# Kernel optimization log

Measured on AMD Instinct MI355X. Metric: run time of the kernel, lower is better.

## Reference

```python
import jax, jax.numpy as jnp
import numpy as np

BETA = 0.25


def setup_inputs() -> dict:
    key = jax.random.key(0)
    k1, k2 = jax.random.split(key)
    z_e = jax.random.normal(k1, (32, 64, 64, 64), dtype=jnp.float32)  # [B, C, W, H]
    # nn.Embedding weight initialized uniform(-1, 1)
    emb = jax.random.uniform(k2, (1024, 64), dtype=jnp.float32, minval=-1.0, maxval=1.0)
    return {"z_e": z_e, "emb": emb}


def reference(z_e, emb):
    B, C, W, H = z_e.shape
    # [B, C, W, H] -> [B, W, H, C] -> [N, C]
    z = jnp.transpose(z_e, (0, 2, 3, 1))
    z_flat = z.reshape(-1, C)  # [N, C]
    # squared euclidean distances: ||z||^2 + ||e||^2 - 2 z e^T  -> [N, K]
    d = (jnp.sum(z_flat ** 2, axis=1, keepdims=True)
         + jnp.sum(emb ** 2, axis=1)
         - 2.0 * jnp.matmul(z_flat, emb.T))
    indices = jnp.argmin(d, axis=1)  # [N]
    quantized = emb[indices].reshape(z.shape)  # [B, W, H, C]
    vq_loss = (jnp.mean((jax.lax.stop_gradient(quantized) - z) ** 2)
               + BETA * jnp.mean((quantized - jax.lax.stop_gradient(z)) ** 2))
    quantized = jnp.transpose(quantized, (0, 3, 1, 2))  # [B, C, W, H]
    return quantized, indices, vq_loss
```

## Files before the change

### kernel.cpp

```cpp
#include <hip/hip_runtime.h>


#define CDIM   64
#define KCODES 1024
#define NPTS   131072
#define WH     4096
#define CWH    262144
#define CTILES (KCODES / 16)
#define DELTA  0.008f

typedef __attribute__((ext_vector_type(4))) float f32x4;
typedef __attribute__((ext_vector_type(8))) short bf16x8;
typedef __attribute__((ext_vector_type(8))) unsigned short u16x8;

__device__ inline unsigned short f2bf(float f) {
    unsigned u = __float_as_uint(f);
    return (unsigned short)((u + 0x7FFFu + ((u >> 16) & 1u)) >> 16);
}
__device__ inline float bf2f(unsigned short h) {
    return __uint_as_float(((unsigned)h) << 16);
}

__global__ __launch_bounds__(256) void vq_prep(const float* __restrict__ emb,
                                               unsigned short* __restrict__ e_swz,
                                               float* __restrict__ E,
                                               int* __restrict__ cnt) {
    const int id = blockIdx.x * 256 + threadIdx.x;
    if (id == 0) cnt[0] = 0;

    if (id < KCODES) {
        const int c = id;
        const float4* e4 = (const float4*)(emb + c * CDIM);
        float s = 0.f;
#pragma unroll
        for (int i = 0; i < CDIM / 4; ++i) {
            float4 v = e4[i];
            s = fmaf(v.x, v.x, s); s = fmaf(v.y, v.y, s);
            s = fmaf(v.z, v.z, s); s = fmaf(v.w, v.w, s);
        }
        E[c] = s;
    }

    if (id < KCODES * 8) {
        const int c  = id >> 3;
        const int kh = (id >> 2) & 1;
        const int g  = id & 3;
        const int ct = c >> 4, col = c & 15;
        const int lane = (g << 4) | col;
        const size_t bh = ((size_t)(ct * 2 + 0) * 2 + kh) * 512 + (size_t)lane * 8;
        const size_t bl = ((size_t)(ct * 2 + 1) * 2 + kh) * 512 + (size_t)lane * 8;
        u16x8 his, los;
#pragma unroll
        for (int j = 0; j < 8; ++j) {
            float v = emb[c * CDIM + kh * 32 + g * 8 + j];
            unsigned short hi = f2bf(v);
            unsigned short lo = f2bf(v - bf2f(hi));
            his[j] = hi;
            los[j] = lo;
        }
        *(u16x8*)&e_swz[bh] = his;
        *(u16x8*)&e_swz[bl] = los;
    }
}

__global__ __launch_bounds__(256) void vq_scan_mfma(const float* __restrict__ z_e,
                                                    const unsigned short* __restrict__ e_swz,
                                                    const float* __restrict__ E,
                                                    int* __restrict__ bestk,
                                                    int* __restrict__ list,
                                                    int* __restrict__ cnt) {
    const int tid = threadIdx.x;
    const int n0  = blockIdx.x * 128;
    const int b   = n0 >> 12;
    const int wh0 = n0 & 4095;

    __shared__ unsigned short zfrag[8][2][2][512];

    const float* zp = z_e + (size_t)b * CWH + wh0;
#pragma unroll 4
    for (int i = 0; i < 32; ++i) {
        int flat = i * 256 + tid;
        int c = flat >> 7, p = flat & 127;
        float v = zp[(size_t)c * WH + p];
        unsigned short hi = f2bf(v);
        unsigned short lo = f2bf(v - bf2f(hi));
        int slot = ((((c & 31) >> 3) << 4) | (p & 15)) * 8 + (c & 7);
        zfrag[p >> 4][0][c >> 5][slot] = hi;
        zfrag[p >> 4][1][c >> 5][slot] = lo;
    }
    __syncthreads();

    const int lane = tid & 63;
    const int w    = tid >> 6;

    bf16x8 zf[2][2][2];
#pragma unroll
    for (int pt = 0; pt < 2; ++pt)
#pragma unroll
        for (int s = 0; s < 2; ++s)
#pragma unroll
            for (int kh = 0; kh < 2; ++kh)
                zf[pt][s][kh] = *(const bf16x8*)&zfrag[2 * w + pt][s][kh][lane * 8];

    const bf16x8* ebv = (const bf16x8*)e_swz;
    const int eoff = ((lane >> 4) << 2);

    float m1a[4], m2a[4], m1b[4], m2b[4];
    int   k1a[4], k1b[4];
#pragma unroll
    for (int i = 0; i < 4; ++i) {
        m1a[i] = 1e30f; m2a[i] = 1e30f; k1a[i] = 0;
        m1b[i] = 1e30f; m2b[i] = 1e30f; k1b[i] = 0;
    }

    bf16x8 eh0 = ebv[0 * 64 + lane];
    bf16x8 eh1 = ebv[1 * 64 + lane];
    bf16x8 el0 = ebv[2 * 64 + lane];
    bf16x8 el1 = ebv[3 * 64 + lane];
    f32x4  Ev  = *(const f32x4*)(E + eoff);

    for (int ct = 0; ct < CTILES; ++ct) {
        const int ctn = (ct + 1) & 63;
        bf16x8 p0 = ebv[(ctn * 4 + 0) * 64 + lane];
        bf16x8 p1 = ebv[(ctn * 4 + 1) * 64 + lane];
        bf16x8 p2 = ebv[(ctn * 4 + 2) * 64 + lane];
        bf16x8 p3 = ebv[(ctn * 4 + 3) * 64 + lane];
        f32x4  Ep = *(const f32x4*)(E + ctn * 16 + eoff);

        f32x4 acc0 = {0.f, 0.f, 0.f, 0.f};
        f32x4 acc1 = {0.f, 0.f, 0.f, 0.f};
        acc0 = __builtin_amdgcn_mfma_f32_16x16x32_bf16(eh0, zf[0][0][0], acc0, 0, 0, 0);
        acc0 = __builtin_amdgcn_mfma_f32_16x16x32_bf16(eh1, zf[0][0][1], acc0, 0, 0, 0);
        acc0 = __builtin_amdgcn_mfma_f32_16x16x32_bf16(eh0, zf[0][1][0], acc0, 0, 0, 0);
        acc0 = __builtin_amdgcn_mfma_f32_16x16x32_bf16(eh1, zf[0][1][1], acc0, 0, 0, 0);
        acc0 = __builtin_amdgcn_mfma_f32_16x16x32_bf16(el0, zf[0][0][0], acc0, 0, 0, 0);
        acc0 = __builtin_amdgcn_mfma_f32_16x16x32_bf16(el1, zf[0][0][1], acc0, 0, 0, 0);
        acc1 = __builtin_amdgcn_mfma_f32_16x16x32_bf16(eh0, zf[1][0][0], acc1, 0, 0, 0);
        acc1 = __builtin_amdgcn_mfma_f32_16x16x32_bf16(eh1, zf[1][0][1], acc1, 0, 0, 0);
        acc1 = __builtin_amdgcn_mfma_f32_16x16x32_bf16(eh0, zf[1][1][0], acc1, 0, 0, 0);
        acc1 = __builtin_amdgcn_mfma_f32_16x16x32_bf16(eh1, zf[1][1][1], acc1, 0, 0, 0);
        acc1 = __builtin_amdgcn_mfma_f32_16x16x32_bf16(el0, zf[1][0][0], acc1, 0, 0, 0);
        acc1 = __builtin_amdgcn_mfma_f32_16x16x32_bf16(el1, zf[1][0][1], acc1, 0, 0, 0);

        const int kb = ct * 16 + eoff;
#pragma unroll
        for (int i = 0; i < 4; ++i) {
            float s0 = fmaf(-2.0f, acc0[i], Ev[i]);
            if (s0 < m1a[i]) { m2a[i] = m1a[i]; m1a[i] = s0; k1a[i] = kb + i; }
            else             { m2a[i] = fminf(m2a[i], s0); }
            float s1 = fmaf(-2.0f, acc1[i], Ev[i]);
            if (s1 < m1b[i]) { m2b[i] = m1b[i]; m1b[i] = s1; k1b[i] = kb + i; }
            else             { m2b[i] = fminf(m2b[i], s1); }
        }

        eh0 = p0; eh1 = p1; el0 = p2; el1 = p3; Ev = Ep;
    }

    float m1A = m1a[0], m2A = m2a[0]; int k1A = k1a[0];
    float m1B = m1b[0], m2B = m2b[0]; int k1B = k1b[0];
#pragma unroll
    for (int i = 1; i < 4; ++i) {
        bool take = (m1a[i] < m1A) || (m1a[i] == m1A && k1a[i] < k1A);
        float nm2 = take ? fminf(m1A, m2a[i]) : fminf(m2A, m1a[i]);
        if (take) { m1A = m1a[i]; k1A = k1a[i]; }
        m2A = nm2;
        take = (m1b[i] < m1B) || (m1b[i] == m1B && k1b[i] < k1B);
        nm2 = take ? fminf(m1B, m2b[i]) : fminf(m2B, m1b[i]);
        if (take) { m1B = m1b[i]; k1B = k1b[i]; }
        m2B = nm2;
    }

#pragma unroll
    for (int d = 16; d <= 32; d <<= 1) {
        float om1 = __shfl_xor(m1A, d); int ok1 = __shfl_xor(k1A, d); float om2 = __shfl_xor(m2A, d);
        bool take = (om1 < m1A) || (om1 == m1A && ok1 < k1A);
        float nm2 = take ? fminf(m1A, om2) : fminf(m2A, om1);
        if (take) { m1A = om1; k1A = ok1; }
        m2A = nm2;
        om1 = __shfl_xor(m1B, d); ok1 = __shfl_xor(k1B, d); om2 = __shfl_xor(m2B, d);
        take = (om1 < m1B) || (om1 == m1B && ok1 < k1B);
        nm2 = take ? fminf(m1B, om2) : fminf(m2B, om1);
        if (take) { m1B = om1; k1B = ok1; }
        m2B = nm2;
    }

    if (lane < 16) {
        int na  = n0 + (2 * w + 0) * 16 + lane;
        int nb_ = n0 + (2 * w + 1) * 16 + lane;
        bestk[na]  = k1A;
        bestk[nb_] = k1B;
        if (m2A - m1A <= DELTA) { int p = atomicAdd(cnt, 1); list[p] = na; }
        if (m2B - m1B <= DELTA) { int p = atomicAdd(cnt, 1); list[p] = nb_; }
    }
}

__global__ __launch_bounds__(256) void vq_rescue(const float* __restrict__ z_e,
                                                 const float* __restrict__ emb,
                                                 const float* __restrict__ E,
                                                 const int* __restrict__ list,
                                                 const int* __restrict__ cnt,
                                                 int* __restrict__ bestk) {
    const int total  = cnt[0];
    const int lane   = threadIdx.x & 63;
    const int wid    = (blockIdx.x * 256 + threadIdx.x) >> 6;
    const int nwaves = (gridDim.x * 256) >> 6;

    for (int i = wid; i < total; i += nwaves) {
        const int n  = list[i];
        const int b  = n >> 12, wh = n & 4095;
        const float* zp = z_e + (size_t)b * CWH + wh;
        float z[CDIM];
#pragma unroll
        for (int c = 0; c < CDIM; ++c) z[c] = zp[c * WH];

        float best = 1e30f; int bk = 0;
        const int kbase = lane * 16;
#pragma unroll 4
        for (int j = 0; j < 16; ++j) {
            const int k = kbase + j;
            const float4* er4 = (const float4*)(emb + k * CDIM);
            float d0 = 0.f, d1 = 0.f, d2 = 0.f, d3 = 0.f;
#pragma unroll
            for (int c4 = 0; c4 < CDIM / 4; ++c4) {
                float4 v = er4[c4];
                d0 = fmaf(z[4 * c4 + 0], v.x, d0);
                d1 = fmaf(z[4 * c4 + 1], v.y, d1);
                d2 = fmaf(z[4 * c4 + 2], v.z, d2);
                d3 = fmaf(z[4 * c4 + 3], v.w, d3);
            }
            float dot   = (d0 + d1) + (d2 + d3);
            float score = fmaf(-2.0f, dot, E[k]);
            if (score < best) { best = score; bk = k; }
        }
#pragma unroll
        for (int d = 1; d < 64; d <<= 1) {
            float ob = __shfl_xor(best, d);
            int   ok = __shfl_xor(bk, d);
            if (ob < best || (ob == best && ok < bk)) { best = ob; bk = ok; }
        }
        if (lane == 0) bestk[n] = bk;
    }
}

__global__ __launch_bounds__(256) void vq_merge(const float* __restrict__ z_e,
                                                const float* __restrict__ emb,
                                                const int* __restrict__ kf,
                                                float* __restrict__ out_q,
                                                float* __restrict__ out_idx,
                                                float* __restrict__ partials) {
    const int tid = threadIdx.x;
    const int cq  = tid >> 5;
    const int pq  = tid & 31;
    const int n0  = blockIdx.x * 128 + pq * 4;
    const int b   = n0 >> 12;
    const int wh  = n0 & 4095;

    const int4 mk4 = *(const int4*)&kf[n0];
    if (cq == 0) {
        float4 fx = { (float)mk4.x, (float)mk4.y, (float)mk4.z, (float)mk4.w };
        *(float4*)&out_idx[n0] = fx;
    }

    const int c0 = cq * 8;
    float4 e0a = *(const float4*)&emb[mk4.x * CDIM + c0];
    float4 e0b = *(const float4*)&emb[mk4.x * CDIM + c0 + 4];
    float4 e1a = *(const float4*)&emb[mk4.y * CDIM + c0];
    float4 e1b = *(const float4*)&emb[mk4.y * CDIM + c0 + 4];
    float4 e2a = *(const float4*)&emb[mk4.z * CDIM + c0];
    float4 e2b = *(const float4*)&emb[mk4.z * CDIM + c0 + 4];
    float4 e3a = *(const float4*)&emb[mk4.w * CDIM + c0];
    float4 e3b = *(const float4*)&emb[mk4.w * CDIM + c0 + 4];

    float qv[8][4];
    qv[0][0] = e0a.x; qv[0][1] = e1a.x; qv[0][2] = e2a.x; qv[0][3] = e3a.x;
    qv[1][0] = e0a.y; qv[1][1] = e1a.y; qv[1][2] = e2a.y; qv[1][3] = e3a.y;
    qv[2][0] = e0a.z; qv[2][1] = e1a.z; qv[2][2] = e2a.z; qv[2][3] = e3a.z;
    qv[3][0] = e0a.w; qv[3][1] = e1a.w; qv[3][2] = e2a.w; qv[3][3] = e3a.w;
    qv[4][0] = e0b.x; qv[4][1] = e1b.x; qv[4][2] = e2b.x; qv[4][3] = e3b.x;
    qv[5][0] = e0b.y; qv[5][1] = e1b.y; qv[5][2] = e2b.y; qv[5][3] = e3b.y;
    qv[6][0] = e0b.z; qv[6][1] = e1b.z; qv[6][2] = e2b.z; qv[6][3] = e3b.z;
    qv[7][0] = e0b.w; qv[7][1] = e1b.w; qv[7][2] = e2b.w; qv[7][3] = e3b.w;

    const float* zb = z_e   + (size_t)b * CWH + wh;
    float*       qb = out_q + (size_t)b * CWH + wh;
    float lsum = 0.f;
#pragma unroll
    for (int cc = 0; cc < 8; ++cc) {
        const int c = c0 + cc;
        float4 z4 = *(const float4*)&zb[(size_t)c * WH];
        float4 q4 = { qv[cc][0], qv[cc][1], qv[cc][2], qv[cc][3] };
        *(float4*)&qb[(size_t)c * WH] = q4;
        float dx = q4.x - z4.x, dy = q4.y - z4.y;
        float dz = q4.z - z4.z, dw = q4.w - z4.w;
        lsum = fmaf(dx, dx, lsum); lsum = fmaf(dy, dy, lsum);
        lsum = fmaf(dz, dz, lsum); lsum = fmaf(dw, dw, lsum);
    }

    __shared__ float red[256];
    red[tid] = lsum;
    __syncthreads();
    for (int s = 128; s > 0; s >>= 1) {
        if (tid < s) red[tid] += red[tid + s];
        __syncthreads();
    }
    if (tid == 0) partials[blockIdx.x] = red[0];
}

__global__ __launch_bounds__(1024) void vq_loss_fin(const float* __restrict__ partials,
                                                    float* __restrict__ loss) {
    __shared__ float red[1024];
    int t = threadIdx.x;
    red[t] = partials[t];
    __syncthreads();
    for (int s = 512; s > 0; s >>= 1) {
        if (t < s) red[t] += red[t + s];
        __syncthreads();
    }
    if (t == 0) loss[0] = red[0] * (1.25f / 8388608.0f);
}

extern "C" void kernel_launch(void* const* d_in, const int* in_sizes, int n_in,
                              void* d_out, int out_size, void* d_ws, size_t ws_size,
                              hipStream_t stream) {
    const float* z_e = (const float*)d_in[0];
    const float* emb = (const float*)d_in[1];

    float* out      = (float*)d_out;
    float* out_q    = out;
    float* out_idx  = out + 8388608;
    float* out_loss = out + 8388608 + 131072;

    char* w = (char*)d_ws;
    float*          E        = (float*)(w);
    unsigned short* e_swz    = (unsigned short*)(w + 4096);
    int*            bestk    = (int*)(w + 266240);
    int*            list     = (int*)(w + 790528);
    int*            cnt      = (int*)(w + 1314816);
    float*          partials = (float*)(w + 1315840);

    vq_prep<<<32, 256, 0, stream>>>(emb, e_swz, E, cnt);
    vq_scan_mfma<<<NPTS / 128, 256, 0, stream>>>(z_e, e_swz, E, bestk, list, cnt);
    vq_rescue<<<2048, 256, 0, stream>>>(z_e, emb, E, list, cnt, bestk);
    vq_merge<<<NPTS / 128, 256, 0, stream>>>(z_e, emb, bestk, out_q, out_idx, partials);
    vq_loss_fin<<<1, 1024, 0, stream>>>(partials, out_loss);
}
```

Measured before the change: 114.7 us.

## Split codebook scan across two grid slices and merge partial minima

The MFMA distance scan now processes half of the codebook per block using a 2D grid, writing per-slice best/second-best distances and indices to workspace. A new finalize kernel merges the two slices, writes the best index and builds the ambiguous-point rescue list. This doubles the number of scan blocks to raise parallelism. In exchange, each z tile is loaded and converted twice, partial results go through global memory, and there is an extra kernel launch.

Measured after the change: 124.8 us. 8.8% more time.

```diff
diff --git a/kernel.cpp b/kernel.cpp
--- a/kernel.cpp
+++ b/kernel.cpp
@@ -6,7 +6,6 @@
 #define NPTS   131072
 #define WH     4096
 #define CWH    262144
-#define CTILES (KCODES / 16)
 #define DELTA  0.008f
 
 typedef __attribute__((ext_vector_type(4))) float f32x4;
@@ -66,11 +65,13 @@
 __global__ __launch_bounds__(256) void vq_scan_mfma(const float* __restrict__ z_e,
                                                     const unsigned short* __restrict__ e_swz,
                                                     const float* __restrict__ E,
-                                                    int* __restrict__ bestk,
-                                                    int* __restrict__ list,
-                                                    int* __restrict__ cnt) {
+                                                    float* __restrict__ cm1,
+                                                    float* __restrict__ cm2,
+                                                    int* __restrict__ ck) {
     const int tid = threadIdx.x;
     const int n0  = blockIdx.x * 128;
+    const int ks  = blockIdx.y;
+    const int ct0 = ks * 32;
     const int b   = n0 >> 12;
     const int wh0 = n0 & 4095;
 
@@ -113,14 +114,15 @@
         m1b[i] = 1e30f; m2b[i] = 1e30f; k1b[i] = 0;
     }
 
-    bf16x8 eh0 = ebv[0 * 64 + lane];
-    bf16x8 eh1 = ebv[1 * 64 + lane];
-    bf16x8 el0 = ebv[2 * 64 + lane];
-    bf16x8 el1 = ebv[3 * 64 + lane];
-    f32x4  Ev  = *(const f32x4*)(E + eoff);
-
-    for (int ct = 0; ct < CTILES; ++ct) {
-        const int ctn = (ct + 1) & 63;
+    bf16x8 eh0 = ebv[(ct0 * 4 + 0) * 64 + lane];
+    bf16x8 eh1 = ebv[(ct0 * 4 + 1) * 64 + lane];
+    bf16x8 el0 = ebv[(ct0 * 4 + 2) * 64 + lane];
+    bf16x8 el1 = ebv[(ct0 * 4 + 3) * 64 + lane];
+    f32x4  Ev  = *(const f32x4*)(E + ct0 * 16 + eoff);
+
+    for (int ctl = 0; ctl < 32; ++ctl) {
+        const int ct  = ct0 + ctl;
+        const int ctn = ct0 + ((ctl + 1) & 31);
         bf16x8 p0 = ebv[(ctn * 4 + 0) * 64 + lane];
         bf16x8 p1 = ebv[(ctn * 4 + 1) * 64 + lane];
         bf16x8 p2 = ebv[(ctn * 4 + 2) * 64 + lane];
@@ -187,11 +189,27 @@
     if (lane < 16) {
         int na  = n0 + (2 * w + 0) * 16 + lane;
         int nb_ = n0 + (2 * w + 1) * 16 + lane;
-        bestk[na]  = k1A;
-        bestk[nb_] = k1B;
-        if (m2A - m1A <= DELTA) { int p = atomicAdd(cnt, 1); list[p] = na; }
-        if (m2B - m1B <= DELTA) { int p = atomicAdd(cnt, 1); list[p] = nb_; }
-    }
+        const int base = ks * NPTS;
+        cm1[base + na]  = m1A; cm2[base + na]  = m2A; ck[base + na]  = k1A;
+        cm1[base + nb_] = m1B; cm2[base + nb_] = m2B; ck[base + nb_] = k1B;
+    }
+}
+
+__global__ __launch_bounds__(256) void vq_finalize(const float* __restrict__ cm1,
+                                                   const float* __restrict__ cm2,
+                                                   const int* __restrict__ ck,
+                                                   int* __restrict__ bestk,
+                                                   int* __restrict__ list,
+                                                   int* __restrict__ cnt) {
+    const int n = blockIdx.x * 256 + threadIdx.x;
+    float a1 = cm1[n],        a2 = cm2[n];        int ak = ck[n];
+    float b1 = cm1[NPTS + n], b2 = cm2[NPTS + n]; int bk = ck[NPTS + n];
+    bool take = (b1 < a1) || (b1 == a1 && bk < ak);
+    float m1 = take ? b1 : a1;
+    int   k1 = take ? bk : ak;
+    float m2 = take ? fminf(a1, b2) : fminf(a2, b1);
+    bestk[n] = k1;
+    if (m2 - m1 <= DELTA) { int p = atomicAdd(cnt, 1); list[p] = n; }
 }
 
 __global__ __launch_bounds__(256) void vq_rescue(const float* __restrict__ z_e,
@@ -335,11 +353,16 @@
     unsigned short* e_swz    = (unsigned short*)(w + 4096);
     int*            bestk    = (int*)(w + 266240);
     int*            list     = (int*)(w + 790528);
-    int*            cnt      = (int*)(w + 1314816);
-    float*          partials = (float*)(w + 1315840);
+    float*          cm1      = (float*)(w + 1314816);
+    float*          cm2      = (float*)(w + 2363392);
+    int*            ck       = (int*)(w + 3411968);
+    int*            cnt      = (int*)(w + 4460544);
+    float*          partials = (float*)(w + 4461568);
 
     vq_prep<<<32, 256, 0, stream>>>(emb, e_swz, E, cnt);
-    vq_scan_mfma<<<NPTS / 128, 256, 0, stream>>>(z_e, e_swz, E, bestk, list, cnt);
+    dim3 gscan(NPTS / 128, 2);
+    vq_scan_mfma<<<gscan, 256, 0, stream>>>(z_e, e_swz, E, cm1, cm2, ck);
+    vq_finalize<<<NPTS / 256, 256, 0, stream>>>(cm1, cm2, ck, bestk, list, cnt);
     vq_rescue<<<2048, 256, 0, stream>>>(z_e, emb, E, list, cnt, bestk);
     vq_merge<<<NPTS / 128, 256, 0, stream>>>(z_e, emb, bestk, out_q, out_idx, partials);
     vq_loss_fin<<<1, 1024, 0, stream>>>(partials, out_loss);
```
